# Kernel tuning notes

Hardware: AMD Instinct MI355X
Metric: run time of the kernel (lower is better)

Reference implementation:

```python
import jax, jax.numpy as jnp
import numpy as np

HEADS = 4
PK = 32  # patch_kernel


def _starts(size, step, d):
    out = []
    for i in range(0, size + step - d, step):
        out.append(min(i, size - d))
    return np.asarray(out)


def dwconv3(x, w, b=None):
    # depthwise 3x3 conv, NCHW, weight (C,1,3,3)
    y = jax.lax.conv_general_dilated(
        x, w, window_strides=(1, 1), padding=((1, 1), (1, 1)),
        dimension_numbers=("NCHW", "OIHW", "NCHW"), feature_group_count=x.shape[1])
    if b is not None:
        y = y + b[None, :, None, None]
    return y


def conv1(x, w):
    # 1x1 conv as channel matmul, weight (O, C)
    return jnp.einsum("bchw,oc->bohw", x, w)


def partition(x, step, d):
    # overlapping windows, matching local_partition (i outer, j inner)
    b, c, h, w = x.shape
    sh = _starts(h, step, d)
    sw = _starts(w, step, d)
    ridx = sh[:, None] + np.arange(d)            # (nh, d)
    cidx = sw[:, None] + np.arange(d)            # (nw, d)
    xw = x[:, :, ridx, :]                        # (b, c, nh, d, w)
    xw = xw[:, :, :, :, cidx]                    # (b, c, nh, d, nw, d)
    xw = jnp.transpose(xw, (0, 2, 4, 1, 3, 5))   # (b, nh, nw, c, d, d)
    return xw.reshape(b, len(sh) * len(sw), c, d, d)


def reverse(shape, win, step, d):
    # overlap-add + count-based averaging, matching local_reverse
    b, c, h, w = shape
    sh = _starts(h, step, d)
    sw = _starts(w, step, d)
    nh, nw = len(sh), len(sw)
    ridx = (sh[:, None] + np.arange(d)).reshape(nh, 1, d, 1)
    cidx = (sw[:, None] + np.arange(d)).reshape(1, nw, 1, d)
    win6 = win.reshape(b, nh, nw, c, d, d).transpose(0, 3, 1, 2, 4, 5)  # (b,c,nh,nw,d,d)
    out = jnp.zeros(shape, win.dtype).at[:, :, ridx, cidx].add(win6)
    cnt = jnp.zeros((h, w), win.dtype).at[ridx, cidx].add(1.0)
    return out / cnt[None, None]


def setup_inputs() -> dict:
    key = jax.random.key(0)
    ks = jax.random.split(key, 9)
    b, dim, Hs, Hx = 2, 128, 62, 248
    s = 0.05
    return {
        "x": jax.random.normal(ks[0], (b, dim, Hx, Hx), jnp.float32),
        "sp": jax.random.normal(ks[1], (b, dim, Hs, Hs), jnp.float32),
        "w_pos": jax.random.normal(ks[2], (dim, 1, 3, 3), jnp.float32) * s,
        "b_pos": jax.random.normal(ks[3], (dim,), jnp.float32) * s,
        "w_q": jax.random.normal(ks[4], (dim, dim), jnp.float32) * s,
        "w_qdw": jax.random.normal(ks[5], (dim, 1, 3, 3), jnp.float32) * s,
        "w_kv": jax.random.normal(ks[6], (2 * dim, dim), jnp.float32) * s,
        "w_kvdw": jax.random.normal(ks[7], (2 * dim, 1, 3, 3), jnp.float32) * s,
        "w_out": jax.random.normal(ks[8], (dim, dim), jnp.float32) * s,
    }


def reference(x, sp, w_pos, b_pos, w_q, w_qdw, w_kv, w_kvdw, w_out):
    p1, p2 = PK, PK // 4               # 32, 8
    s1, s2 = p1 - p1 // 4, p2 - p2 // 4  # 24, 6
    x = x + dwconv3(x, w_pos, b_pos)
    sp = sp + dwconv3(sp, w_pos, b_pos)
    q = dwconv3(conv1(sp, w_q), w_qdw)      # (b, c, Hs, Ws)
    kv = dwconv3(conv1(x, w_kv), w_kvdw)    # (b, 2c, Hx, Wx)
    qw = partition(q, s2, p2)               # (b, n, c, 8, 8)
    kvw = partition(kv, s1, p1)             # (b, n, 2c, 32, 32)
    kw, vw = jnp.split(kvw, 2, axis=2)
    b, n, c = qw.shape[0], qw.shape[1], qw.shape[2]
    hd = c // HEADS

    def to_heads(t, d):  # 'b n (head c) dh dw -> (b n) head (dh dw) c'
        return t.reshape(b * n, HEADS, hd, d * d).transpose(0, 1, 3, 2)

    qh, kh, vh = to_heads(qw, p2), to_heads(kw, p1), to_heads(vw, p1)
    attn = jax.nn.softmax(jnp.einsum("bhqc,bhkc->bhqk", qh, kh) * (hd ** -0.5), axis=-1)
    out = jnp.einsum("bhqk,bhkc->bhqc", attn, vh)
    out = out.transpose(0, 1, 3, 2).reshape(b, n, c, p2, p2)
    out = reverse(sp.shape, out, s2, p2)
    return conv1(out, w_out)
```

## Files before the change

### kernel.cpp

```cpp
#include <hip/hip_runtime.h>
#include <cstdint>

#define HS 62
#define HX 248
#define HXW (HX * HX)
#define HSW (HS * HS)
#define HXP 256
#define HXWP (HX * HXP)

typedef __attribute__((ext_vector_type(8))) short bf16x8;
typedef __attribute__((ext_vector_type(4))) float f32x4;
typedef __attribute__((ext_vector_type(2))) float f32x2;

static __device__ __forceinline__ unsigned short f2bf(float f) {
  uint32_t u = __builtin_bit_cast(uint32_t, f);
  u += 0x7fff + ((u >> 16) & 1);
  return (unsigned short)(u >> 16);
}
static __device__ __forceinline__ float bf2f(unsigned short u) {
  uint32_t x = (uint32_t)u << 16;
  return __builtin_bit_cast(float, x);
}

static __device__ __forceinline__ void pkfma(f32x2& acc, f32x2 a, f32x2 b) {
  asm("v_pk_fma_f32 %0, %1, %2, %0" : "+v"(acc) : "v"(a), "v"(b));
}
static __device__ __forceinline__ uint32_t cvtpk(float lo, float hi) {
  uint32_t r;
  asm("v_cvt_pk_bf16_f32 %0, %1, %2" : "=v"(r) : "v"(lo), "v"(hi));
  return r;
}
static __device__ __forceinline__ f32x2 unp(uint32_t u) {
  f32x2 r;
  r.x = __builtin_bit_cast(float, u << 16);
  r.y = __builtin_bit_cast(float, u & 0xffff0000u);
  return r;
}


static __device__ void dwconv8x2_body(const float* __restrict__ x,
                                      const float* __restrict__ w,
                                      const float* __restrict__ bias,
                                      unsigned short* __restrict__ y, int i) {
  int wq = (i % 31) * 8;
  int t = i / 31;
  int hp = t % 124;
  int bc = t / 124;
  int c = bc & 127;
  int hy = hp * 2;
  const float* xb = x + (size_t)bc * HXW;
  const float* wc = w + c * 9;
  float bv = bias[c];

  float rm1[10], r0[10], r1[10], r2[10];
  auto loadrow = [&](int h2, float (&r)[10]) {
    const float* row = xb + (size_t)h2 * HX + wq;
    float4 a = *(const float4*)row;
    float4 b2 = *(const float4*)(row + 4);
    r[1] = a.x;  r[2] = a.y;  r[3] = a.z;  r[4] = a.w;
    r[5] = b2.x; r[6] = b2.y; r[7] = b2.z; r[8] = b2.w;
    r[0] = (wq > 0) ? row[-1] : 0.0f;
    r[9] = (wq + 8 < HX) ? row[8] : 0.0f;
  };
  loadrow((hy > 0) ? hy - 1 : 0, rm1);
  loadrow(hy, r0);
  loadrow(hy + 1, r1);
  loadrow((hy + 2 < HX) ? hy + 2 : HX - 1, r2);
  if (hp == 0) {
#pragma unroll
    for (int k = 0; k < 10; k++) rm1[k] = 0.0f;
  }
  if (hp == 123) {
#pragma unroll
    for (int k = 0; k < 10; k++) r2[k] = 0.0f;
  }

  float w0 = wc[0], w1 = wc[1], w2 = wc[2];
  float w3 = wc[3], w4 = wc[4], w5 = wc[5];
  float w6 = wc[6], w7 = wc[7], w8 = wc[8];

  float o0[8], o1[8];
#pragma unroll
  for (int k = 0; k < 8; k++) {
    float s = bv;
    s += w0 * rm1[k]; s += w1 * rm1[k + 1]; s += w2 * rm1[k + 2];
    s += w3 * r0[k];  s += w4 * r0[k + 1];  s += w5 * r0[k + 2];
    s += w6 * r1[k];  s += w7 * r1[k + 1];  s += w8 * r1[k + 2];
    o0[k] = s + r0[k + 1];
    float u = bv;
    u += w0 * r0[k]; u += w1 * r0[k + 1]; u += w2 * r0[k + 2];
    u += w3 * r1[k]; u += w4 * r1[k + 1]; u += w5 * r1[k + 2];
    u += w6 * r2[k]; u += w7 * r2[k + 1]; u += w8 * r2[k + 2];
    o1[k] = u + r1[k + 1];
  }
  uint4 d0, d1;
  d0.x = cvtpk(o0[0], o0[1]); d0.y = cvtpk(o0[2], o0[3]);
  d0.z = cvtpk(o0[4], o0[5]); d0.w = cvtpk(o0[6], o0[7]);
  d1.x = cvtpk(o1[0], o1[1]); d1.y = cvtpk(o1[2], o1[3]);
  d1.z = cvtpk(o1[4], o1[5]); d1.w = cvtpk(o1[6], o1[7]);
  unsigned short* yb = y + (size_t)bc * HXW + (size_t)hy * HX + wq;
  *(uint4*)yb = d0;
  *(uint4*)(yb + HX) = d1;
}

static __device__ void dwconv3sp_body(const float* __restrict__ x,
                                      const float* __restrict__ w,
                                      const float* __restrict__ bias,
                                      float* __restrict__ y, int i) {
  int wx = i % HS;
  int t = i / HS;
  int hy = t % HS;
  int bc = t / HS;
  int c = bc & 127;
  const float* xb = x + (size_t)bc * HSW;
  const float* wc = w + c * 9;
  float s = bias[c];
  for (int di = -1; di <= 1; di++) {
    int h2 = hy + di;
    if (h2 < 0 || h2 >= HS) continue;
    for (int dj = -1; dj <= 1; dj++) {
      int w2 = wx + dj;
      if (w2 < 0 || w2 >= HS) continue;
      s += xb[(size_t)h2 * HS + w2] * wc[(di + 1) * 3 + (dj + 1)];
    }
  }
  s += xb[(size_t)hy * HS + wx];
  y[i] = s;
}

static __device__ void dwconv_q_body(const float* __restrict__ x,
                                     const float* __restrict__ w,
                                     unsigned short* __restrict__ qn, int i) {
  int wx = i % HS;
  int t = i / HS;
  int hy = t % HS;
  int bc = t / HS;
  int c = bc & 127;
  int b = bc >> 7;
  const float* xb = x + (size_t)bc * HSW;
  const float* wc = w + c * 9;
  float s = 0.0f;
  for (int di = -1; di <= 1; di++) {
    int h2 = hy + di;
    if (h2 < 0 || h2 >= HS) continue;
    for (int dj = -1; dj <= 1; dj++) {
      int w2 = wx + dj;
      if (w2 < 0 || w2 >= HS) continue;
      s += xb[(size_t)h2 * HS + w2] * wc[(di + 1) * 3 + (dj + 1)];
    }
  }
  qn[((size_t)(b * HSW + hy * HS + wx)) * 128 + c] = f2bf(s * 0.17677669529663688f);
}

static __device__ void conv1_kv_body(const unsigned short* __restrict__ xpb,
                                     const unsigned short* __restrict__ wkb,
                                     unsigned short* __restrict__ y,
                                     int bx, int b, char* smem) {
  unsigned short* bufA = (unsigned short*)smem;
  unsigned short* bufW = bufA + 64 * 136;
  int p0 = bx * 64;
  int tid = threadIdx.x;
  int wave = tid >> 6, lane = tid & 63, quad = lane >> 4, l15 = lane & 15;

  {
    int c = tid >> 1, half = tid & 1;
    const unsigned short* src = xpb + ((size_t)(b * 128 + c)) * HXW + p0 + half * 32;
#pragma unroll
    for (int j = 0; j < 8; j++) {
      uint2 v = *(const uint2*)(src + j * 4);
      int px = half * 32 + j * 4;
      bufA[(px + 0) * 136 + c] = (unsigned short)(v.x & 0xffff);
      bufA[(px + 1) * 136 + c] = (unsigned short)(v.x >> 16);
      bufA[(px + 2) * 136 + c] = (unsigned short)(v.y & 0xffff);
      bufA[(px + 3) * 136 + c] = (unsigned short)(v.y >> 16);
    }
  }
  __syncthreads();
  bf16x8 A[4];
#pragma unroll
  for (int kb = 0; kb < 4; kb++)
    A[kb] = __builtin_bit_cast(bf16x8,
        *(const uint4*)&bufA[(wave * 16 + l15) * 136 + kb * 32 + quad * 8]);

  const f32x4 zf = {0.f, 0.f, 0.f, 0.f};
#pragma unroll 1
  for (int h = 0; h < 2; h++) {
#pragma unroll 1
    for (int oq = 0; oq < 2; oq++) {
      __syncthreads();
      {
        int orow = tid >> 2;
        int cseg = (tid & 3) * 32;
        const unsigned short* src = wkb + (size_t)(h * 128 + oq * 64 + orow) * 128 + cseg;
        unsigned short* dst = &bufW[orow * 136 + cseg];
        *(uint4*)(dst)      = *(const uint4*)(src);
        *(uint4*)(dst + 8)  = *(const uint4*)(src + 8);
        *(uint4*)(dst + 16) = *(const uint4*)(src + 16);
        *(uint4*)(dst + 24) = *(const uint4*)(src + 24);
      }
      __syncthreads();
#pragma unroll
      for (int ot = 0; ot < 4; ot++) {
        const unsigned short* wrow = &bufW[(ot * 16 + l15) * 136 + quad * 8];
        f32x4 D = zf;
        D = __builtin_amdgcn_mfma_f32_16x16x32_bf16(A[0], __builtin_bit_cast(bf16x8, *(const uint4*)(wrow)),      D, 0, 0, 0);
        D = __builtin_amdgcn_mfma_f32_16x16x32_bf16(A[1], __builtin_bit_cast(bf16x8, *(const uint4*)(wrow + 32)), D, 0, 0, 0);
        D = __builtin_amdgcn_mfma_f32_16x16x32_bf16(A[2], __builtin_bit_cast(bf16x8, *(const uint4*)(wrow + 64)), D, 0, 0, 0);
        D = __builtin_amdgcn_mfma_f32_16x16x32_bf16(A[3], __builtin_bit_cast(bf16x8, *(const uint4*)(wrow + 96)), D, 0, 0, 0);
#pragma unroll
        for (int r = 0; r < 4; r++)
          bufA[(wave * 16 + quad * 4 + r) * 136 + (oq * 4 + ot) * 16 + l15] = f2bf(D[r]);
      }
    }
    __syncthreads();
    {
      int px = tid >> 2, og = (tid & 3) * 32;
      const uint4* srcp = (const uint4*)&bufA[px * 136 + og];
      uint4* dstp = (uint4*)(y + ((size_t)b * HXW + p0 + px) * 256 + h * 128 + og);
#pragma unroll
      for (int j = 0; j < 4; j++) dstp[j] = srcp[j];
    }
  }
}

static __device__ void conv1_body(const float* __restrict__ x,
                                  const float* __restrict__ w,
                                  float* __restrict__ y, int HW, int O,
                                  int bx, int by, int bz, char* smem) {
  constexpr int K = 128;
  constexpr int BK = 32;
  float (*ws_s)[64] = (float(*)[64])smem;
  float (*xs_s)[64] = (float(*)[64])(smem + BK * 64 * sizeof(float));
  int b = bz;
  int o0 = by * 64;
  int p0 = bx * 64;
  const float* xb = x + (size_t)b * K * HW;
  int tx = threadIdx.x & 15;
  int ty = threadIdx.x >> 4;
  float acc[4][4] = {};
  int lo = threadIdx.x >> 2;
  int lk = (threadIdx.x & 3) * 8;
  int lc = threadIdx.x >> 3;
  int lp = (threadIdx.x & 7) * 8;

  for (int k0 = 0; k0 < K; k0 += BK) {
    __syncthreads();
    {
      const float* wp = w + (size_t)(o0 + lo) * K + k0 + lk;
      float4 a = *(const float4*)wp;
      float4 bq = *(const float4*)(wp + 4);
      ws_s[lk + 0][lo] = a.x;  ws_s[lk + 1][lo] = a.y;
      ws_s[lk + 2][lo] = a.z;  ws_s[lk + 3][lo] = a.w;
      ws_s[lk + 4][lo] = bq.x; ws_s[lk + 5][lo] = bq.y;
      ws_s[lk + 6][lo] = bq.z; ws_s[lk + 7][lo] = bq.w;
    }
    {
      int p = p0 + lp;
      const float* xp = xb + (size_t)(k0 + lc) * HW;
      float4 a, bq;
      if (p + 7 < HW) {
        a = *(const float4*)(xp + p);
        bq = *(const float4*)(xp + p + 4);
      } else {
        float tv[8];
#pragma unroll
        for (int j = 0; j < 8; j++) tv[j] = (p + j < HW) ? xp[p + j] : 0.0f;
        a = make_float4(tv[0], tv[1], tv[2], tv[3]);
        bq = make_float4(tv[4], tv[5], tv[6], tv[7]);
      }
      *(float4*)&xs_s[lc][lp] = a;
      *(float4*)&xs_s[lc][lp + 4] = bq;
    }
    __syncthreads();
#pragma unroll
    for (int k = 0; k < BK; k++) {
      float4 wv = *(const float4*)&ws_s[k][ty * 4];
      float4 xv = *(const float4*)&xs_s[k][tx * 4];
      acc[0][0] += wv.x * xv.x; acc[0][1] += wv.x * xv.y; acc[0][2] += wv.x * xv.z; acc[0][3] += wv.x * xv.w;
      acc[1][0] += wv.y * xv.x; acc[1][1] += wv.y * xv.y; acc[1][2] += wv.y * xv.z; acc[1][3] += wv.y * xv.w;
      acc[2][0] += wv.z * xv.x; acc[2][1] += wv.z * xv.y; acc[2][2] += wv.z * xv.z; acc[2][3] += wv.z * xv.w;
      acc[3][0] += wv.w * xv.x; acc[3][1] += wv.w * xv.y; acc[3][2] += wv.w * xv.z; acc[3][3] += wv.w * xv.w;
    }
  }
  int p = p0 + tx * 4;
  float* yb = y + (size_t)b * O * HW + (size_t)(o0 + ty * 4) * HW;
#pragma unroll
  for (int j = 0; j < 4; j++) {
    float* yr = yb + (size_t)j * HW + p;
    if (p + 3 < HW) {
      *(float4*)yr = make_float4(acc[j][0], acc[j][1], acc[j][2], acc[j][3]);
    } else {
#pragma unroll
      for (int e = 0; e < 4; e++) if (p + e < HW) yr[e] = acc[j][e];
    }
  }
}

template <bool VT, bool VB>
static __device__ __forceinline__ void dwkv_rowpair(
    const unsigned short* __restrict__ rm1, const unsigned short* __restrict__ r0,
    const unsigned short* __restrict__ r1, const unsigned short* __restrict__ r2,
    const f32x2 (&wp)[9], int px0, f32x2 (&a0)[8], f32x2 (&a1)[8]) {
  const f32x2 z2 = {0.f, 0.f};
#pragma unroll
  for (int p = 0; p < 8; p++) { a0[p] = z2; a1[p] = z2; }
#pragma unroll
  for (int j = 0; j < 10; j++) {
    int xcol = px0 - 1 + j;
    int xc = xcol;
    if (j == 0) xc = (xcol < 0) ? 0 : xcol;
    if (j == 9) xc = (xcol > HX - 1) ? HX - 1 : xcol;
    size_t off = (size_t)xc * 256;
    uint32_t um1 = 0, u0, u1, u2 = 0;
    u0 = *(const uint32_t*)(r0 + off);
    u1 = *(const uint32_t*)(r1 + off);
    if constexpr (VT) um1 = *(const uint32_t*)(rm1 + off);
    if constexpr (VB) u2 = *(const uint32_t*)(r2 + off);
    if (j == 0 || j == 9) {
      bool oob = (j == 0) ? (xcol < 0) : (xcol > HX - 1);
      if (oob) { um1 = 0u; u0 = 0u; u1 = 0u; u2 = 0u; }
    }
    f32x2 dm1, d0 = unp(u0), d1 = unp(u1), d2;
    if constexpr (VT) dm1 = unp(um1);
    if constexpr (VB) d2 = unp(u2);
    if (j <= 7) {
      if constexpr (VT) pkfma(a0[j], wp[0], dm1);
      pkfma(a0[j], wp[3], d0);
      pkfma(a0[j], wp[6], d1);
      pkfma(a1[j], wp[0], d0);
      pkfma(a1[j], wp[3], d1);
      if constexpr (VB) pkfma(a1[j], wp[6], d2);
    }
    if (j >= 1 && j <= 8) {
      if constexpr (VT) pkfma(a0[j - 1], wp[1], dm1);
      pkfma(a0[j - 1], wp[4], d0);
      pkfma(a0[j - 1], wp[7], d1);
      pkfma(a1[j - 1], wp[1], d0);
      pkfma(a1[j - 1], wp[4], d1);
      if constexpr (VB) pkfma(a1[j - 1], wp[7], d2);
    }
    if (j >= 2) {
      if constexpr (VT) pkfma(a0[j - 2], wp[2], dm1);
      pkfma(a0[j - 2], wp[5], d0);
      pkfma(a0[j - 2], wp[8], d1);
      pkfma(a1[j - 2], wp[2], d0);
      pkfma(a1[j - 2], wp[5], d1);
      if constexpr (VB) pkfma(a1[j - 2], wp[8], d2);
    }
  }
}

#define VTS 72
#define VTROW (128 * VTS + 16)

static __device__ void dwconv_kv_body(const unsigned short* __restrict__ tkv,
                                      const float* __restrict__ w,
                                      unsigned short* __restrict__ kT,
                                      unsigned short* __restrict__ vv,
                                      int fid, int b, unsigned short* vt) {
  int xcd = fid & 7, slot = fid >> 3;
  int gi = xcd * 62 + slot;
  int strip = gi / 124;
  int g = gi % 124;
  int x0 = strip * 64;
  int tid = threadIdx.x;
  int cl = tid & 127;
  int pg = tid >> 7;
  int ch0 = cl * 2;
  int hy0 = g * 2;

  f32x2 wp[9];
#pragma unroll
  for (int t = 0; t < 9; t++) {
    wp[t].x = w[ch0 * 9 + t];
    wp[t].y = w[(ch0 + 1) * 9 + t];
  }

  const unsigned short* r0 = tkv + (size_t)b * HXW * 256 + (size_t)hy0 * (HX * 256) + ch0;
  const unsigned short* r1 = r0 + HX * 256;
  const unsigned short* rm1 = r0 - HX * 256;
  const unsigned short* r2 = r1 + HX * 256;
  bool isK = (cl < 64);
  int c0 = ch0 - 128;

#pragma unroll 1
  for (int half = 0; half < 2; half++) {
    int px0 = x0 + pg * 16 + half * 8;
    if (px0 < HX) {
      f32x2 a0[8], a1[8];
      if (g == 0)        dwkv_rowpair<false, true >(rm1, r0, r1, r2, wp, px0, a0, a1);
      else if (g == 123) dwkv_rowpair<true,  false>(rm1, r0, r1, r2, wp, px0, a0, a1);
      else               dwkv_rowpair<true,  true >(rm1, r0, r1, r2, wp, px0, a0, a1);

      if (isK) {
        unsigned short* kb0 = kT + ((size_t)b * HXW + (size_t)hy0 * HX + px0) * 128 + ch0;
        unsigned short* kb1 = kb0 + (size_t)HX * 128;
#pragma unroll
        for (int p = 0; p < 8; p++) {
          *(uint32_t*)(kb0 + (size_t)p * 128) = cvtpk(a0[p].x, a0[p].y);
          *(uint32_t*)(kb1 + (size_t)p * 128) = cvtpk(a1[p].x, a1[p].y);
        }
      } else {
        int pxr = pg * 16 + half * 8;
        unsigned short* v0 = vt + c0 * VTS + pxr;
        unsigned short* v1 = v0 + VTS;
        uint2 d;
        d.x = cvtpk(a0[0].x, a0[1].x); d.y = cvtpk(a0[2].x, a0[3].x);
        *(uint2*)(v0) = d;
        d.x = cvtpk(a0[4].x, a0[5].x); d.y = cvtpk(a0[6].x, a0[7].x);
        *(uint2*)(v0 + 4) = d;
        d.x = cvtpk(a0[0].y, a0[1].y); d.y = cvtpk(a0[2].y, a0[3].y);
        *(uint2*)(v1) = d;
        d.x = cvtpk(a0[4].y, a0[5].y); d.y = cvtpk(a0[6].y, a0[7].y);
        *(uint2*)(v1 + 4) = d;
        d.x = cvtpk(a1[0].x, a1[1].x); d.y = cvtpk(a1[2].x, a1[3].x);
        *(uint2*)(v0 + VTROW) = d;
        d.x = cvtpk(a1[4].x, a1[5].x); d.y = cvtpk(a1[6].x, a1[7].x);
        *(uint2*)(v0 + VTROW + 4) = d;
        d.x = cvtpk(a1[0].y, a1[1].y); d.y = cvtpk(a1[2].y, a1[3].y);
        *(uint2*)(v1 + VTROW) = d;
        d.x = cvtpk(a1[4].y, a1[5].y); d.y = cvtpk(a1[6].y, a1[7].y);
        *(uint2*)(v1 + VTROW + 4) = d;
      }
    }
  }
  __syncthreads();
  {
    int ch = tid >> 2;
    int row = (tid >> 1) & 1;
    int ph = (tid & 1) * 32;
    const unsigned short* srcv = vt + row * VTROW + ch * VTS + ph;
    unsigned short* dst = vv + (size_t)(b * 128 + ch) * HXWP + (size_t)(hy0 + row) * HXP + x0 + ph;
#pragma unroll
    for (int j = 0; j < 4; j++)
      *(uint4*)(dst + j * 8) = *(const uint4*)(srcv + j * 8);
  }
}

#define NB_DW8 3844
#define NB_DW3 3844
#define NB_CVT 128

__global__ __launch_bounds__(256) void comboA_kernel(
    const float* __restrict__ x, const float* __restrict__ w_pos,
    const float* __restrict__ b_pos, unsigned short* __restrict__ xpb,
    const float* __restrict__ sp, float* __restrict__ spp,
    const float* __restrict__ w_kv, unsigned short* __restrict__ wkb) {
  int bid = blockIdx.x, tid = threadIdx.x;
  if (bid < NB_DW8) {
    int i = bid * 256 + tid;
    dwconv8x2_body(x, w_pos, b_pos, xpb, i);
  } else if (bid < NB_DW8 + NB_DW3) {
    int i = (bid - NB_DW8) * 256 + tid;
    dwconv3sp_body(sp, w_pos, b_pos, spp, i);
  } else {
    int i = (bid - NB_DW8 - NB_DW3) * 256 + tid;
    if (i < 32768) wkb[i] = f2bf(w_kv[i]);
  }
}

__global__ __launch_bounds__(256) void comboB_kernel(
    const unsigned short* __restrict__ xpb, const unsigned short* __restrict__ wkb,
    unsigned short* __restrict__ tkv,
    const float* __restrict__ spp, const float* __restrict__ w_q,
    float* __restrict__ tq) {
  __shared__ __align__(16) char smem[64 * 136 * 2 * 2];
  int bid = blockIdx.x;
  if (bid < 1922) {
    conv1_kv_body(xpb, wkb, tkv, bid % 961, bid / 961, smem);
  } else {
    int cid = bid - 1922;
    conv1_body(spp, w_q, tq, HSW, 128, cid % 61, (cid / 61) % 2, cid / 122, smem);
  }
}

__global__ __launch_bounds__(512) __attribute__((amdgpu_waves_per_eu(4)))
void comboC_kernel(const unsigned short* __restrict__ tkv,
                   const float* __restrict__ w_kvdw,
                   unsigned short* __restrict__ kT, unsigned short* __restrict__ vv,
                   const float* __restrict__ tq, const float* __restrict__ w_qdw,
                   unsigned short* __restrict__ qn) {
  __shared__ __align__(16) unsigned short vt[2 * VTROW];
  int bid = blockIdx.x;
  if (bid < 992) {
    dwconv_kv_body(tkv, w_kvdw, kT, vv, bid % 496, bid / 496, vt);
  } else {
    int i = (bid - 992) * 512 + threadIdx.x;
    if (i < 2 * 128 * HSW) dwconv_q_body(tq, w_qdw, qn, i);
  }
}

__global__ __launch_bounds__(256) void conv1_out_kernel(const float* __restrict__ x,
                                                        const float* __restrict__ w,
                                                        float* __restrict__ y, int HW) {
  __shared__ __align__(16) char smem[2 * 32 * 64 * 4];
  conv1_body(x, w, y, HW, 128, blockIdx.x, blockIdx.y, blockIdx.z, smem);
}

__global__ __launch_bounds__(256) void attn_mfma_kernel(
    const unsigned short* __restrict__ qn,
    const unsigned short* __restrict__ kT,
    const unsigned short* __restrict__ vp,
    float* __restrict__ o) {
  int fid = blockIdx.x;
  int xcd = fid & 7, slot = fid >> 3;
  int lin = xcd * 100 + slot;
  int n = lin % 100;
  int bh = lin / 100;
  int h = bh & 3, b = bh >> 2;
  int wi = n / 10, wj = n % 10;
  int wave = threadIdx.x >> 6;
  int oct = wave;
  int lane = threadIdx.x & 63;
  int quad = lane >> 4;
  int l15 = lane & 15;
  int y0 = 24 * wi, x0 = 24 * wj;

  __shared__ __align__(16) unsigned short lds[16896];
  unsigned short* Pw = lds + wave * 2560;

  bf16x8 QB[4];
#pragma unroll
  for (int nt = 0; nt < 4; nt++) {
    int qq = nt * 16 + l15;
    int qy = 6 * wi + (qq >> 3), qx = 6 * wj + (qq & 7);
    QB[nt] = __builtin_bit_cast(bf16x8,
        *(const uint4*)(qn + ((size_t)(b * HSW + qy * HS + qx)) * 128 + h * 32 + quad * 8));
  }

  f32x4 Oacc[2][4];
#pragma unroll
  for (int a = 0; a < 2; a++)
#pragma unroll
    for (int c = 0; c < 4; c++) Oacc[a][c] = f32x4{0.f, 0.f, 0.f, 0.f};
  float lsum[4] = {0.f, 0.f, 0.f, 0.f};

  const unsigned short* kb = kT + (size_t)b * HXW * 128 + h * 32;
  const unsigned short* vb = vp + ((size_t)(b * 128 + h * 32)) * HXWP;
  const f32x4 zf = {0.f, 0.f, 0.f, 0.f};

#define LOADROW(r, K0, K1, V0, V1)                                              \
  {                                                                             \
    int y = y0 + (r);                                                           \
    const unsigned short* krow = kb + ((size_t)(y * HX + x0)) * 128;            \
    K0 = *(const uint4*)(krow + (size_t)l15 * 128 + quad * 8);                  \
    K1 = *(const uint4*)(krow + (size_t)(16 + l15) * 128 + quad * 8);           \
    const unsigned short* vrow = vb + (size_t)y * HXP + x0 + quad * 8;          \
    V0 = *(const uint4*)(vrow + (size_t)l15 * HXWP);                            \
    V1 = *(const uint4*)(vrow + (size_t)(16 + l15) * HXWP);                     \
  }

  auto compute = [&](uint4 k0, uint4 k1, uint4 v0, uint4 v1) {
    bf16x8 KA0 = __builtin_bit_cast(bf16x8, k0);
    bf16x8 KA1 = __builtin_bit_cast(bf16x8, k1);
    bf16x8 VA0 = __builtin_bit_cast(bf16x8, v0);
    bf16x8 VA1 = __builtin_bit_cast(bf16x8, v1);
    f32x4 S[2][4];
#pragma unroll
    for (int nt = 0; nt < 4; nt++) {
      S[0][nt] = __builtin_amdgcn_mfma_f32_16x16x32_bf16(KA0, QB[nt], zf, 0, 0, 0);
      S[1][nt] = __builtin_amdgcn_mfma_f32_16x16x32_bf16(KA1, QB[nt], zf, 0, 0, 0);
    }
#pragma unroll
    for (int nt = 0; nt < 4; nt++) {
      float pv[2][4];
      float cs = 0.f;
#pragma unroll
      for (int mt = 0; mt < 2; mt++)
#pragma unroll
        for (int r = 0; r < 4; r++) {
          pv[mt][r] = __expf(S[mt][nt][r]);
          cs += pv[mt][r];
        }
      lsum[nt] += cs;
#pragma unroll
      for (int mt = 0; mt < 2; mt++) {
        uint2 d;
        d.x = (uint32_t)f2bf(pv[mt][0]) | ((uint32_t)f2bf(pv[mt][1]) << 16);
        d.y = (uint32_t)f2bf(pv[mt][2]) | ((uint32_t)f2bf(pv[mt][3]) << 16);
        *(uint2*)(Pw + (16 * nt + l15) * 40 + 16 * mt + quad * 4) = d;
      }
    }
#pragma unroll
    for (int nt = 0; nt < 4; nt++) {
      bf16x8 PB = __builtin_bit_cast(bf16x8, *(const uint4*)(Pw + (16 * nt + l15) * 40 + quad * 8));
      Oacc[0][nt] = __builtin_amdgcn_mfma_f32_16x16x32_bf16(VA0, PB, Oacc[0][nt], 0, 0, 0);
      Oacc[1][nt] = __builtin_amdgcn_mfma_f32_16x16x32_bf16(VA1, PB, Oacc[1][nt], 0, 0, 0);
    }
  };

  int rbase = oct * 8;
  uint4 kA0, kA1, vA0, vA1, kB0, kB1, vB0, vB1;
  LOADROW(rbase + 0, kA0, kA1, vA0, vA1);
  LOADROW(rbase + 1, kB0, kB1, vB0, vB1);
#pragma unroll 1
  for (int r = 0; r < 8; r += 2) {
    compute(kA0, kA1, vA0, vA1);
    {
      int rn = (r + 2 < 8) ? (r + 2) : 6;
      LOADROW(rbase + rn, kA0, kA1, vA0, vA1);
    }
    compute(kB0, kB1, vB0, vB1);
    {
      int rn = (r + 3 < 8) ? (r + 3) : 7;
      LOADROW(rbase + rn, kB0, kB1, vB0, vB1);
    }
  }
#undef LOADROW

#pragma unroll
  for (int nt = 0; nt < 4; nt++) {
    lsum[nt] += __shfl_xor(lsum[nt], 16, 64);
    lsum[nt] += __shfl_xor(lsum[nt], 32, 64);
  }

  float* mO = (float*)lds;
  float* mL = (float*)(lds + 16384);
  __syncthreads();
#pragma unroll
  for (int mt = 0; mt < 2; mt++)
#pragma unroll
    for (int nt = 0; nt < 4; nt++)
#pragma unroll
      for (int r = 0; r < 4; r++)
        mO[oct * 2048 + (16 * mt + quad * 4 + r) * 64 + 16 * nt + l15] = Oacc[mt][nt][r];
  if (quad == 0) {
#pragma unroll
    for (int nt = 0; nt < 4; nt++) mL[oct * 64 + nt * 16 + l15] = lsum[nt];
  }
  __syncthreads();
  {
    int q = threadIdx.x & 63;
    int cg = threadIdx.x >> 6;
    float inv = 1.0f / (mL[q] + mL[64 + q] + mL[128 + q] + mL[192 + q]);
    float* ob = o + (((size_t)(b * 100 + n)) * 128 + h * 32 + cg * 8) * 64 + q;
#pragma unroll
    for (int e = 0; e < 8; e++) {
      int ch = cg * 8 + e;
      float s = mO[ch * 64 + q] + mO[2048 + ch * 64 + q] +
                mO[4096 + ch * 64 + q] + mO[6144 + ch * 64 + q];
      ob[(size_t)e * 64] = s * inv;
    }
  }
}

__global__ void reverse_kernel(const float* __restrict__ win, float* __restrict__ out) {
  int i = blockIdx.x * 256 + threadIdx.x;
  const int total = 2 * 128 * HSW;
  if (i >= total) return;
  int x = i % HS;
  int t = i / HS;
  int y = t % HS;
  t /= HS;
  int c = t % 128;
  int b = t / 128;
  int wi0 = (y >= 7) ? (y - 2) / 6 : 0;
  int wi1 = min(9, y / 6);
  int wj0 = (x >= 7) ? (x - 2) / 6 : 0;
  int wj1 = min(9, x / 6);
  float s = 0.0f;
  for (int wi = wi0; wi <= wi1; wi++)
    for (int wj = wj0; wj <= wj1; wj++) {
      int di = y - 6 * wi, dj = x - 6 * wj;
      s += win[(((size_t)(b * 100 + wi * 10 + wj)) * 128 + c) * 64 + di * 8 + dj];
    }
  float cnt = (float)((wi1 - wi0 + 1) * (wj1 - wj0 + 1));
  out[i] = s / cnt;
}

extern "C" void kernel_launch(void* const* d_in, const int* in_sizes, int n_in,
                              void* d_out, int out_size, void* d_ws, size_t ws_size,
                              hipStream_t stream) {
  const float* x      = (const float*)d_in[0];
  const float* sp     = (const float*)d_in[1];
  const float* w_pos  = (const float*)d_in[2];
  const float* b_pos  = (const float*)d_in[3];
  const float* w_q    = (const float*)d_in[4];
  const float* w_qdw  = (const float*)d_in[5];
  const float* w_kv   = (const float*)d_in[6];
  const float* w_kvdw = (const float*)d_in[7];
  const float* w_out  = (const float*)d_in[8];
  float* out = (float*)d_out;

  const size_t N_x   = (size_t)2 * 128 * HXW;
  const size_t N_vp  = (size_t)2 * 128 * HXWP;
  const size_t N_s   = (size_t)2 * 128 * HSW;
  const size_t N_att = (size_t)2 * 100 * 128 * 64;

  float* ws = (float*)d_ws;
  unsigned short* xpb = (unsigned short*)ws;
  unsigned short* kT  = (unsigned short*)ws;
  unsigned short* vv  = kT + N_x;
  unsigned short* tkv = vv + N_vp;
  float* att = (float*)tkv;
  float* rev = att + N_att;
  float* spp = (float*)(tkv + 2 * N_x);
  float* tq  = spp + N_s;
  unsigned short* qn  = (unsigned short*)(tq + N_s);
  unsigned short* wkb = qn + N_s;
  (void)ws_size; (void)in_sizes; (void)n_in; (void)out_size;

  comboA_kernel<<<NB_DW8 + NB_DW3 + NB_CVT, 256, 0, stream>>>(
      x, w_pos, b_pos, xpb, sp, spp, w_kv, wkb);
  comboB_kernel<<<1922 + 244, 256, 0, stream>>>(xpb, wkb, tkv, spp, w_q, tq);
  comboC_kernel<<<992 + 1922, 512, 0, stream>>>(tkv, w_kvdw, kT, vv, tq, w_qdw, qn);
  attn_mfma_kernel<<<800, 256, 0, stream>>>(qn, kT, vv, att);
  {
    int total = (int)N_s;
    reverse_kernel<<<(total + 255) / 256, 256, 0, stream>>>(att, rev);
  }
  {
    dim3 grid((HSW + 63) / 64, 2, 2);
    conv1_out_kernel<<<grid, 256, 0, stream>>>(rev, w_out, out, HSW);
  }
}
```

Baseline: 252.0 us.

## Prepack kv weights into MFMA fragment layout and swizzle LDS staging

Weights for the kv 1x1 conv are converted to bf16 and packed once into per-lane MFMA B-fragment order. Each wave then reads its B operands straight from global memory into registers, with a software prefetch of the next tile, instead of staging weights through LDS with extra barriers. The activation transpose into LDS now uses wide 16-byte loads across four channels, packed 8-byte stores and an XOR swizzle to cut bank conflicts. LDS use is halved, which may allow more resident blocks, in exchange for more register pressure and redundant global and L2 reads of the weights across blocks.

```diff
diff --git a/kernel.cpp b/kernel.cpp
--- a/kernel.cpp
+++ b/kernel.cpp
@@ -152,74 +152,108 @@
   qn[((size_t)(b * HSW + hy * HS + wx)) * 128 + c] = f2bf(s * 0.17677669529663688f);
 }
 
+static __device__ void pack_wfrag_body(const float* __restrict__ w_kv,
+                                       unsigned short* __restrict__ wf, int i) {
+  int lane = i & 63;
+  int f = i >> 6;
+  int hq = f >> 4, ot = (f >> 2) & 3, kb = f & 3;
+  int l15 = lane & 15, quad = lane >> 4;
+  const float* src = w_kv + (size_t)(hq * 64 + ot * 16 + l15) * 128 + kb * 32 + quad * 8;
+  unsigned short* dst = wf + (size_t)i * 8;
+#pragma unroll
+  for (int j = 0; j < 8; j++) dst[j] = f2bf(src[j]);
+}
+
 static __device__ void conv1_kv_body(const unsigned short* __restrict__ xpb,
-                                     const unsigned short* __restrict__ wkb,
+                                     const unsigned short* __restrict__ wf,
                                      unsigned short* __restrict__ y,
                                      int bx, int b, char* smem) {
   unsigned short* bufA = (unsigned short*)smem;
-  unsigned short* bufW = bufA + 64 * 136;
   int p0 = bx * 64;
   int tid = threadIdx.x;
   int wave = tid >> 6, lane = tid & 63, quad = lane >> 4, l15 = lane & 15;
 
   {
-    int c = tid >> 1, half = tid & 1;
-    const unsigned short* src = xpb + ((size_t)(b * 128 + c)) * HXW + p0 + half * 32;
-#pragma unroll
-    for (int j = 0; j < 8; j++) {
-      uint2 v = *(const uint2*)(src + j * 4);
-      int px = half * 32 + j * 4;
-      bufA[(px + 0) * 136 + c] = (unsigned short)(v.x & 0xffff);
-      bufA[(px + 1) * 136 + c] = (unsigned short)(v.x >> 16);
-      bufA[(px + 2) * 136 + c] = (unsigned short)(v.y & 0xffff);
-      bufA[(px + 3) * 136 + c] = (unsigned short)(v.y >> 16);
+    int pxg = (tid & 7) * 8;
+    int c0 = (tid >> 3) * 4;
+    const unsigned short* src = xpb + ((size_t)(b * 128 + c0)) * HXW + p0 + pxg;
+    uint4 r0 = *(const uint4*)(src);
+    uint4 r1 = *(const uint4*)(src + (size_t)HXW);
+    uint4 r2 = *(const uint4*)(src + 2 * (size_t)HXW);
+    uint4 r3 = *(const uint4*)(src + 3 * (size_t)HXW);
+    const uint32_t* q0 = (const uint32_t*)&r0;
+    const uint32_t* q1 = (const uint32_t*)&r1;
+    const uint32_t* q2 = (const uint32_t*)&r2;
+    const uint32_t* q3 = (const uint32_t*)&r3;
+    int swz = (tid & 7) << 3;
+    int cs = c0 ^ swz;
+#pragma unroll
+    for (int p = 0; p < 4; p++) {
+      uint32_t d0 = q0[p], d1 = q1[p], d2 = q2[p], d3 = q3[p];
+      uint2 wlo, whi;
+      wlo.x = (d0 & 0xffffu) | (d1 << 16);
+      wlo.y = (d2 & 0xffffu) | (d3 << 16);
+      whi.x = (d0 >> 16) | (d1 & 0xffff0000u);
+      whi.y = (d2 >> 16) | (d3 & 0xffff0000u);
+      *(uint2*)&bufA[(pxg + 2 * p) * 136 + cs] = wlo;
+      *(uint2*)&bufA[(pxg + 2 * p + 1) * 136 + cs] = whi;
     }
   }
   __syncthreads();
+
   bf16x8 A[4];
-#pragma unroll
-  for (int kb = 0; kb < 4; kb++)
-    A[kb] = __builtin_bit_cast(bf16x8,
-        *(const uint4*)&bufA[(wave * 16 + l15) * 136 + kb * 32 + quad * 8]);
+  {
+    int px = wave * 16 + l15;
+    int swz = ((px >> 3) & 7) << 3;
+#pragma unroll
+    for (int kb = 0; kb < 4; kb++)
+      A[kb] = __builtin_bit_cast(bf16x8,
+          *(const uint4*)&bufA[px * 136 + ((kb * 32 + quad * 8) ^ swz)]);
+  }
 
   const f32x4 zf = {0.f, 0.f, 0.f, 0.f};
+  const uint4* wfu = (const uint4*)wf;
+  uint4 Bc[4], Bn[4];
+  {
+    const uint4* fb = wfu + lane;
+    Bc[0] = fb[0]; Bc[1] = fb[64]; Bc[2] = fb[128]; Bc[3] = fb[192];
+  }
+  int orow = wave * 16 + quad * 4;
 #pragma unroll 1
   for (int h = 0; h < 2; h++) {
-#pragma unroll 1
-    for (int oq = 0; oq < 2; oq++) {
-      __syncthreads();
-      {
-        int orow = tid >> 2;
-        int cseg = (tid & 3) * 32;
-        const unsigned short* src = wkb + (size_t)(h * 128 + oq * 64 + orow) * 128 + cseg;
-        unsigned short* dst = &bufW[orow * 136 + cseg];
-        *(uint4*)(dst)      = *(const uint4*)(src);
-        *(uint4*)(dst + 8)  = *(const uint4*)(src + 8);
-        *(uint4*)(dst + 16) = *(const uint4*)(src + 16);
-        *(uint4*)(dst + 24) = *(const uint4*)(src + 24);
+#pragma unroll
+    for (int tt = 0; tt < 8; tt++) {
+      int t = h * 8 + tt;
+      if (t < 15) {
+        const uint4* fb = wfu + (size_t)(t + 1) * 256 + lane;
+        Bn[0] = fb[0]; Bn[1] = fb[64]; Bn[2] = fb[128]; Bn[3] = fb[192];
       }
-      __syncthreads();
-#pragma unroll
-      for (int ot = 0; ot < 4; ot++) {
-        const unsigned short* wrow = &bufW[(ot * 16 + l15) * 136 + quad * 8];
-        f32x4 D = zf;
-        D = __builtin_amdgcn_mfma_f32_16x16x32_bf16(A[0], __builtin_bit_cast(bf16x8, *(const uint4*)(wrow)),      D, 0, 0, 0);
-        D = __builtin_amdgcn_mfma_f32_16x16x32_bf16(A[1], __builtin_bit_cast(bf16x8, *(const uint4*)(wrow + 32)), D, 0, 0, 0);
-        D = __builtin_amdgcn_mfma_f32_16x16x32_bf16(A[2], __builtin_bit_cast(bf16x8, *(const uint4*)(wrow + 64)), D, 0, 0, 0);
-        D = __builtin_amdgcn_mfma_f32_16x16x32_bf16(A[3], __builtin_bit_cast(bf16x8, *(const uint4*)(wrow + 96)), D, 0, 0, 0);
-#pragma unroll
-        for (int r = 0; r < 4; r++)
-          bufA[(wave * 16 + quad * 4 + r) * 136 + (oq * 4 + ot) * 16 + l15] = f2bf(D[r]);
+      f32x4 D = zf;
+      D = __builtin_amdgcn_mfma_f32_16x16x32_bf16(A[0], __builtin_bit_cast(bf16x8, Bc[0]), D, 0, 0, 0);
+      D = __builtin_amdgcn_mfma_f32_16x16x32_bf16(A[1], __builtin_bit_cast(bf16x8, Bc[1]), D, 0, 0, 0);
+      D = __builtin_amdgcn_mfma_f32_16x16x32_bf16(A[2], __builtin_bit_cast(bf16x8, Bc[2]), D, 0, 0, 0);
+      D = __builtin_amdgcn_mfma_f32_16x16x32_bf16(A[3], __builtin_bit_cast(bf16x8, Bc[3]), D, 0, 0, 0);
+      int col = tt * 16 + l15;
+#pragma unroll
+      for (int r = 0; r < 4; r++) {
+        int row = orow + r;
+        bufA[row * 136 + (col ^ (((row >> 3) & 7) << 3))] = f2bf(D[r]);
+      }
+      if (t < 15) {
+#pragma unroll
+        for (int k = 0; k < 4; k++) Bc[k] = Bn[k];
       }
     }
     __syncthreads();
     {
       int px = tid >> 2, og = (tid & 3) * 32;
-      const uint4* srcp = (const uint4*)&bufA[px * 136 + og];
+      int swz = ((px >> 3) & 7) << 3;
       uint4* dstp = (uint4*)(y + ((size_t)b * HXW + p0 + px) * 256 + h * 128 + og);
 #pragma unroll
-      for (int j = 0; j < 4; j++) dstp[j] = srcp[j];
-    }
+      for (int j = 0; j < 4; j++)
+        dstp[j] = *(const uint4*)&bufA[px * 136 + ((og + j * 8) ^ swz)];
+    }
+    __syncthreads();
   }
 }
 
@@ -439,7 +473,7 @@
 
 #define NB_DW8 3844
 #define NB_DW3 3844
-#define NB_CVT 128
+#define NB_PKW 16
 
 __global__ __launch_bounds__(256) void comboA_kernel(
     const float* __restrict__ x, const float* __restrict__ w_pos,
@@ -455,7 +489,7 @@
     dwconv3sp_body(sp, w_pos, b_pos, spp, i);
   } else {
     int i = (bid - NB_DW8 - NB_DW3) * 256 + tid;
-    if (i < 32768) wkb[i] = f2bf(w_kv[i]);
+    if (i < 4096) pack_wfrag_body(w_kv, wkb, i);
   }
 }
 
@@ -464,7 +498,7 @@
     unsigned short* __restrict__ tkv,
     const float* __restrict__ spp, const float* __restrict__ w_q,
     float* __restrict__ tq) {
-  __shared__ __align__(16) char smem[64 * 136 * 2 * 2];
+  __shared__ __align__(16) char smem[64 * 136 * 2];
   int bid = blockIdx.x;
   if (bid < 1922) {
     conv1_kv_body(xpb, wkb, tkv, bid % 961, bid / 961, smem);
@@ -700,7 +734,7 @@
   unsigned short* wkb = qn + N_s;
   (void)ws_size; (void)in_sizes; (void)n_in; (void)out_size;
 
-  comboA_kernel<<<NB_DW8 + NB_DW3 + NB_CVT, 256, 0, stream>>>(
+  comboA_kernel<<<NB_DW8 + NB_DW3 + NB_PKW, 256, 0, stream>>>(
       x, w_pos, b_pos, xpb, sp, spp, w_kv, wkb);
   comboB_kernel<<<1922 + 244, 256, 0, stream>>>(xpb, wkb, tkv, spp, w_q, tq);
   comboC_kernel<<<992 + 1922, 512, 0, stream>>>(tkv, w_kvdw, kT, vv, tq, w_qdw, qn);
```

Result: no change. 257.0 us (+2.0%).
